# Performance work log

Hardware: AMD Instinct MI355X
Metric: run time of the kernel (lower is better)

The kernel has to match this reference:

```python
import jax, jax.numpy as jnp
import numpy as np

# smoothing constants (from init_kwargs)
KERNEL_SIZE = 20
WINDOW = (-10.0, 10.0)
SIGMA = 4.0
AMPLITUDE = 0.5
N_SMOOTH = 331  # 350 - 20 + 1


def setup_inputs() -> dict:
    key = jax.random.key(0)
    ks = jax.random.split(key, 6)
    W, A, M, D = 4000, 64, 6, 500
    wavelengths = jnp.linspace(0.3, 2.5, W, dtype=jnp.float32)  # um
    grid = jnp.linspace(0.25, 2.6, D, dtype=jnp.float32)        # material wavelength tables
    n_tab = 1.3 + 1.5 * jax.random.uniform(ks[0], (M, D), dtype=jnp.float32)
    k_tab = 0.05 * jax.random.uniform(ks[1], (M, D), dtype=jnp.float32)
    fixed_data = jnp.stack([jnp.broadcast_to(grid, (M, D)), n_tab, k_tab], axis=1)  # [M,3,D]
    refractive_index = 1.5 + 1.5 * jax.random.uniform(ks[2], (350,), dtype=jnp.float32)
    compression_ratio = jnp.ones((1,), jnp.float32)
    thickness_above_unk = 0.05 + 0.2 * jax.random.uniform(ks[3], (10,), dtype=jnp.float32)  # um
    thickness_below_unk = 0.05 + 0.2 * jax.random.uniform(ks[4], (9,), dtype=jnp.float32)   # um
    angle_of_incidences = jnp.linspace(0.0, 60.0, A, dtype=jnp.float32)  # degrees
    # stack order: incoming | 10 above | unknown (index M) | 9 below | outgoing
    md = [0] + [1, 2] * 5 + [M] + [3, 4] * 4 + [3] + [5]
    material_distribution = jnp.array(md, dtype=jnp.int32)  # [22]
    unknown_layer_thickness = jnp.array([500.0], jnp.float32)  # nm
    return dict(refractive_index=refractive_index, compression_ratio=compression_ratio,
                fixed_data=fixed_data, thickness_above_unk=thickness_above_unk,
                thickness_below_unk=thickness_below_unk, wavelengths=wavelengths,
                angle_of_incidences=angle_of_incidences,
                material_distribution=material_distribution, polarization=0,
                unknown_layer_thickness=unknown_layer_thickness)


def reference(refractive_index, compression_ratio, fixed_data, thickness_above_unk,
              thickness_below_unk, wavelengths, angle_of_incidences,
              material_distribution, polarization, unknown_layer_thickness):
    D = fixed_data.shape[2]
    n_repeat = D - N_SMOOTH
    # --- gaussian smoothing of the unknown layer's refractive index (valid conv) ---
    x = jnp.linspace(WINDOW[0], WINDOW[1], KERNEL_SIZE)
    g = AMPLITUDE * jnp.exp(-0.5 * (x / SIGMA) ** 2)
    g = (g / jnp.sum(g)).astype(refractive_index.dtype)
    nk_s = jnp.convolve(refractive_index, g, mode='valid')            # [331]
    nk = jnp.concatenate([nk_s, jnp.full((n_repeat,), nk_s[-1], nk_s.dtype)])  # pad to max_data_dim
    dyn_wl = jnp.linspace(jnp.min(wavelengths), jnp.max(wavelengths), N_SMOOTH)
    dyn_wl = jnp.concatenate([dyn_wl, jnp.full((n_repeat,), dyn_wl[-1], dyn_wl.dtype)])
    # --- interpolate all material n,k tables onto the experimental wavelengths ---
    interp = jax.vmap(lambda xp, fp: jnp.interp(wavelengths, xp, fp))
    n_fixc = interp(fixed_data[:, 0], fixed_data[:, 1]) + 1j * interp(fixed_data[:, 0], fixed_data[:, 2])  # [M,W]
    n_unk = jnp.interp(wavelengths, dyn_wl, nk)[None].astype(n_fixc.dtype)  # unknown layer (k=0)
    n_mat = jnp.concatenate([n_fixc, n_unk], axis=0)                  # [M+1, W]
    n_stack = n_mat[material_distribution]                            # [Lyr, W] complex
    # --- thickness list (unknown in nm -> um, scaled by compression ratio) ---
    d_unk = unknown_layer_thickness / 1000.0 * compression_ratio      # [1]
    d = jnp.concatenate([thickness_above_unk, d_unk, thickness_below_unk])  # [L] = [20]
    # --- coherent TMM, vectorized over (angle, wavelength) ---
    th0 = jnp.deg2rad(angle_of_incidences)                            # [A]
    sin0 = (n_stack[0][None, :] * jnp.sin(th0)[:, None])              # [A,W] (Snell invariant)
    sin_th = sin0[None] / n_stack[:, None, :]                         # [Lyr,A,W]
    cos_th = jnp.sqrt(1.0 - sin_th ** 2)
    kz = 2.0 * jnp.pi * n_stack[:, None, :] * cos_th / wavelengths[None, None, :]
    delta = kz[1:-1] * d[:, None, None].astype(kz.dtype)              # [L,A,W]
    nc = n_stack[:, None, :]
    if polarization == 0:  # s-pol
        f = nc * cos_th                                               # [Lyr,A,W]
        r = (f[:-1] - f[1:]) / (f[:-1] + f[1:])                       # [L+1,A,W]
        t = 2.0 * f[:-1] / (f[:-1] + f[1:])
    else:  # p-pol
        num = nc[1:] * cos_th[:-1]
        den = nc[:-1] * cos_th[1:]
        r = (num - den) / (num + den)
        t = 2.0 * nc[:-1, ] * cos_th[:-1] / (num + den)
    # Mtilde = I_0 * prod_j (P_j @ I_j); 2x2 complex recursion via scan
    m00 = 1.0 / t[0]
    m01 = r[0] / t[0]
    m10 = m01
    m11 = m00

    def step(carry, xs):
        c00, c01, c10, c11 = carry
        dl, rj, tj = xs
        em = jnp.exp(-1j * dl) / tj
        ep = jnp.exp(1j * dl) / tj
        a, b, c, dd = em, rj * em, rj * ep, ep
        return (c00 * a + c01 * c, c00 * b + c01 * dd,
                c10 * a + c11 * c, c10 * b + c11 * dd), None

    (m00, m01, m10, m11), _ = jax.lax.scan(step, (m00, m01, m10, m11), (delta, r[1:], t[1:]))
    rr = m10 / m00
    tt = 1.0 / m00
    R = jnp.abs(rr) ** 2                                              # [A,W]
    if polarization == 0:
        f0 = n_stack[0][None] * cos_th[0]
        ff = n_stack[-1][None] * cos_th[-1]
        T = jnp.abs(tt) ** 2 * jnp.real(ff) / jnp.real(f0)
    else:
        T = (jnp.abs(tt) ** 2 * jnp.real(n_stack[-1][None] * jnp.conj(cos_th[-1]))
             / jnp.real(n_stack[0][None] * jnp.conj(cos_th[0])))
    Aabs = 1.0 - R - T
    return jnp.stack([R, T, Aabs])  # [3, A, W]
```

## Files before the change

kernel.cpp:

```cpp
#include <hip/hip_runtime.h>

#define DEV __device__ __forceinline__
#define RCP(x)  __builtin_amdgcn_rcpf(x)
#define SQRT(x) __builtin_amdgcn_sqrtf(x)

constexpr int W_  = 4000;
constexpr int A_  = 64;
constexpr int D_  = 500;
constexpr int NS_ = 331;
constexpr int KS_ = 20;
constexpr int L_  = 22;
constexpr float PIF = 3.14159265358979323846f;

struct cplx { float re, im; };

DEV cplx cmul(cplx a, cplx b) { return { a.re*b.re - a.im*b.im, a.re*b.im + a.im*b.re }; }
DEV cplx cinv(cplx z) {
  float d = RCP(fmaf(z.re, z.re, z.im * z.im));
  return { z.re * d, -z.im * d };
}
DEV cplx csqrtc(cplx z) {
  float x = z.re, y = z.im;
  float mag = SQRT(fmaf(x, x, y * y));
  float t   = SQRT(0.5f * (mag + fabsf(x)));
  float q   = y * 0.5f * RCP(t);
  bool pos  = (x >= 0.0f);
  float re  = pos ? t : fabsf(q);
  float im  = pos ? q : copysignf(t, y);
  return { re, im };
}

__global__ __launch_bounds__(256) void precompute_kernel(
    const float* __restrict__ ri,
    const float* __restrict__ fixed,
    const float* __restrict__ wl,
    const int*   __restrict__ md,
    float4* __restrict__ nz)
{
  __shared__ float s_grid[D_];
  __shared__ float s_ri[350];
  __shared__ float s_g[KS_];
  __shared__ float s_mn[4], s_mx[4];

  const int tid = threadIdx.x;

  for (int i = tid; i < D_;  i += 256) s_grid[i] = fixed[i];
  for (int i = tid; i < 350; i += 256) s_ri[i]   = ri[i];
  if (tid < KS_) {
    float x  = -10.0f + (float)tid * (20.0f / 19.0f);
    float xs = x * 0.25f;
    s_g[tid] = 0.5f * expf(-0.5f * xs * xs);
  }

  float lmin = 3.4e38f, lmax = -3.4e38f;
  for (int i = tid; i < W_; i += 256) {
    float v = wl[i];
    lmin = fminf(lmin, v); lmax = fmaxf(lmax, v);
  }
  #pragma unroll
  for (int o = 32; o; o >>= 1) {
    lmin = fminf(lmin, __shfl_xor(lmin, o, 64));
    lmax = fmaxf(lmax, __shfl_xor(lmax, o, 64));
  }
  if ((tid & 63) == 0) { s_mn[tid >> 6] = lmin; s_mx[tid >> 6] = lmax; }
  __syncthreads();
  const float wmin = fminf(fminf(s_mn[0], s_mn[1]), fminf(s_mn[2], s_mn[3]));
  const float wmax = fmaxf(fmaxf(s_mx[0], s_mx[1]), fmaxf(s_mx[2], s_mx[3]));

  const int w  = blockIdx.x * 256 + tid;
  const int wc = min(w, W_ - 1);
  const float x = wl[wc];

  cplx nm[7];

  int lo = 0, hi = D_;
  while (lo < hi) { int mid = (lo + hi) >> 1; if (s_grid[mid] <= x) lo = mid + 1; else hi = mid; }
  const int i = min(max(lo, 1), D_ - 1);
  const float gx0 = s_grid[i - 1];
  const float fr  = (x - gx0) * RCP(s_grid[i] - gx0);
  const bool lowc  = (x < s_grid[0]);
  const bool highc = (x > s_grid[D_ - 1]);

  #pragma unroll
  for (int m = 0; m < 6; ++m) {
    const float* nptr = fixed + (m * 3 + 1) * D_;
    const float* kptr = fixed + (m * 3 + 2) * D_;
    float nv = fmaf(fr, nptr[i] - nptr[i - 1], nptr[i - 1]);
    float kv = fmaf(fr, kptr[i] - kptr[i - 1], kptr[i - 1]);
    if (lowc)  { nv = nptr[0];      kv = kptr[0]; }
    if (highc) { nv = nptr[D_ - 1]; kv = kptr[D_ - 1]; }
    nm[m] = { nv, kv };
  }

  {
    float gsum = 0.0f;
    #pragma unroll
    for (int k = 0; k < KS_; ++k) gsum += s_g[k];
    const float ginv  = 1.0f / gsum;
    const float stepd = (wmax - wmin) / (float)(NS_ - 1);
    int j = (int)floorf((x - wmin) * RCP(stepd)) + 1;
    j = min(max(j, 1), NS_ - 1);
    const int j0 = j - 1;
    float a0 = 0.0f, a1 = 0.0f;
    #pragma unroll
    for (int k = 0; k < KS_; ++k) {
      const float gk = s_g[KS_ - 1 - k];
      a0 = fmaf(s_ri[j0 + k], gk, a0);
      a1 = fmaf(s_ri[j0 + 1 + k], gk, a1);
    }
    a0 *= ginv; a1 *= ginv;
    const float d0 = fmaf((float)j0, stepd, wmin);
    const float d1 = fmaf((float)j,  stepd, wmin);
    nm[6] = { fmaf((x - d0) * RCP(d1 - d0), a1 - a0, a0), 0.0f };
  }

  const int m0 = md[0];
  cplx n0 = nm[0];
  #pragma unroll
  for (int m = 1; m < 7; ++m) if (m0 == m) n0 = nm[m];

  if (w < W_) {
    #pragma unroll
    for (int m = 0; m < 7; ++m) {
      const cplx q = cmul(n0, cinv(nm[m]));
      const cplx z = cmul(q, q);
      nz[m * W_ + w] = make_float4(nm[m].re, nm[m].im, z.re, z.im);
    }
  }
}

__global__ __launch_bounds__(256) void tmm_kernel(
    const float4* __restrict__ nz,
    const float*  __restrict__ wl,
    const float*  __restrict__ ang,
    const int*    __restrict__ md,
    const float*  __restrict__ tha,
    const float*  __restrict__ thb,
    const float*  __restrict__ unk,
    const float*  __restrict__ comp,
    float* __restrict__ out)
{
  __shared__ float4 s_f[7 * 256];

  const int tid = threadIdx.x;
  const int w = blockIdx.x * 256 + tid;
  if (w >= W_) return;
  const int a = blockIdx.y;

  const float th0  = ang[a] * (PIF / 180.0f);
  const float s0   = sinf(th0);
  const float s0sq = s0 * s0;
  const float klam = 2.0f * PIF * RCP(wl[w]);

  #pragma unroll
  for (int m = 0; m < 7; ++m) {
    const float4 v = nz[m * W_ + w];
    const cplx st2 = { v.z * s0sq, v.w * s0sq };
    const cplx ct  = csqrtc({ 1.0f - st2.re, -st2.im });
    const cplx f   = cmul({ v.x, v.y }, ct);
    const cplx fi  = cinv(f);
    s_f[m * 256 + tid] = make_float4(f.re, f.im, fi.re, fi.im);
  }

  cplx u   = { 0.0f, 0.0f };
  cplx tac = { 1.0f, 0.0f };
  float4 fdn = s_f[md[L_ - 1] * 256 + tid];
  const float fL_re = fdn.x;

  #pragma unroll
  for (int j = L_ - 2; j >= 1; --j) {
    const float4 fj = s_f[md[j] * 256 + tid];
    const cplx q   = cmul({ fdn.x, fdn.y }, { fj.z, fj.w });
    const cplx iop = cinv({ 1.0f + q.re, q.im });
    const cplx r   = cmul({ 1.0f - q.re, -q.im }, iop);

    const float dthj = (j - 1) < 10 ? tha[j - 1]
                     : ((j - 1) == 10 ? unk[0] / 1000.0f * comp[0]
                                      : thb[j - 12]);
    const float cst = klam * dthj;
    const float dr = fj.x * cst, di = fj.y * cst;
    const float e2 = __expf(-di);
    float sn, cs;
    __sincosf(dr, &sn, &cs);
    const cplx ph   = { e2 * cs, e2 * sn };
    const cplx beta = cmul(ph, ph);

    const cplx ru  = cmul(r, u);
    const cplx idn = cinv({ 1.0f + ru.re, ru.im });
    tac = cmul(tac, cmul(cmul(iop, ph), idn));
    u = cmul(beta, cmul({ r.re + u.re, r.im + u.im }, idn));

    fdn = fj;
  }

  const float4 f0v = s_f[md[0] * 256 + tid];
  const cplx q0   = cmul({ fdn.x, fdn.y }, { f0v.z, f0v.w });
  const cplx iop0 = cinv({ 1.0f + q0.re, q0.im });
  const cplx r0   = cmul({ 1.0f - q0.re, -q0.im }, iop0);
  const cplx ru0  = cmul(r0, u);
  const cplx idn0 = cinv({ 1.0f + ru0.re, ru0.im });
  const cplx rr   = cmul({ r0.re + u.re, r0.im + u.im }, idn0);
  cplx tt = cmul(cmul(iop0, idn0), tac);

  const float SC = 2097152.0f;
  tt.re *= SC; tt.im *= SC;

  const float R = fmaf(rr.re, rr.re, rr.im * rr.im);
  const float T = fmaf(tt.re, tt.re, tt.im * tt.im) * fL_re * RCP(f0v.x);

  const int o = a * W_ + w;
  out[o]               = R;
  out[A_ * W_ + o]     = T;
  out[2 * A_ * W_ + o] = 1.0f - R - T;
}

extern "C" void kernel_launch(void* const* d_in, const int* in_sizes, int n_in,
                              void* d_out, int out_size, void* d_ws, size_t ws_size,
                              hipStream_t stream) {
  const float* ri    = (const float*)d_in[0];
  const float* comp  = (const float*)d_in[1];
  const float* fixed = (const float*)d_in[2];
  const float* tha   = (const float*)d_in[3];
  const float* thb   = (const float*)d_in[4];
  const float* wl    = (const float*)d_in[5];
  const float* ang   = (const float*)d_in[6];
  const int*   md    = (const int*)d_in[7];
  const float* unk   = (const float*)d_in[9];
  float* out = (float*)d_out;

  float4* nz = (float4*)d_ws;

  precompute_kernel<<<16, 256, 0, stream>>>(ri, fixed, wl, md, nz);
  dim3 grid(16, A_);
  tmm_kernel<<<grid, 256, 0, stream>>>(nz, wl, ang, md, tha, thb, unk, comp, out);
}
```

Baseline: 93.04 us.

## Replace per-layer complex division recursion with projective numerator/denominator form

Reformulates the backward reflection recursion so that reflection is carried as a numerator/denominator pair instead of dividing at each layer. This removes one complex inverse per layer. The transmission phase is accumulated as a sum of exponents and applied once at the end, and the interface factors are accumulated in two interleaved products to shorten the dependency chain. The trade is more complex multiplies per layer, plus magnitude scaling tricks that keep the unnormalized numerator and denominator from overflowing, which carries some numerical range risk.

```diff
diff --git a/kernel.cpp b/kernel.cpp
--- a/kernel.cpp
+++ b/kernel.cpp
@@ -15,6 +15,7 @@
 struct cplx { float re, im; };
 
 DEV cplx cmul(cplx a, cplx b) { return { a.re*b.re - a.im*b.im, a.re*b.im + a.im*b.re }; }
+DEV cplx cadd(cplx a, cplx b) { return { a.re + b.re, a.im + b.im }; }
 DEV cplx cinv(cplx z) {
   float d = RCP(fmaf(z.re, z.re, z.im * z.im));
   return { z.re * d, -z.im * d };
@@ -162,8 +163,10 @@
     s_f[m * 256 + tid] = make_float4(f.re, f.im, fi.re, fi.im);
   }
 
-  cplx u   = { 0.0f, 0.0f };
-  cplx tac = { 1.0f, 0.0f };
+  cplx N  = { 0.0f, 0.0f };
+  cplx Dn = { 1.0f, 0.0f };
+  cplx Pa = { 1.0f, 0.0f }, Pb = { 1.0f, 0.0f };
+  float sdr = 0.0f, sabs = 0.0f;
   float4 fdn = s_f[md[L_ - 1] * 256 + tid];
   const float fL_re = fdn.x;
 
@@ -179,16 +182,21 @@
                                       : thb[j - 12]);
     const float cst = klam * dthj;
     const float dr = fj.x * cst, di = fj.y * cst;
-    const float e2 = __expf(-di);
-    float sn, cs;
-    __sincosf(dr, &sn, &cs);
-    const cplx ph   = { e2 * cs, e2 * sn };
-    const cplx beta = cmul(ph, ph);
-
-    const cplx ru  = cmul(r, u);
-    const cplx idn = cinv({ 1.0f + ru.re, ru.im });
-    tac = cmul(tac, cmul(cmul(iop, ph), idn));
-    u = cmul(beta, cmul({ r.re + u.re, r.im + u.im }, idn));
+    sdr += dr; sabs += fabsf(di);
+    const float em = __expf(-2.0f * fabsf(di));
+    const bool dpos = (di >= 0.0f);
+    const float eN = dpos ? em : 1.0f;
+    const float eD = dpos ? 1.0f : em;
+    float sb, cb;
+    __sincosf(2.0f * dr, &sb, &cb);
+    const cplx pN = { eN * cb, eN * sb };
+
+    if (j & 1) Pa = cmul(Pa, iop); else Pb = cmul(Pb, iop);
+
+    const cplx rN = cmul(r, N);
+    const cplx rD = cmul(r, Dn);
+    N  = cmul(pN, cadd(rD, N));
+    Dn = { eD * (Dn.re + rN.re), eD * (Dn.im + rN.im) };
 
     fdn = fj;
   }
@@ -197,13 +205,21 @@
   const cplx q0   = cmul({ fdn.x, fdn.y }, { f0v.z, f0v.w });
   const cplx iop0 = cinv({ 1.0f + q0.re, q0.im });
   const cplx r0   = cmul({ 1.0f - q0.re, -q0.im }, iop0);
-  const cplx ru0  = cmul(r0, u);
-  const cplx idn0 = cinv({ 1.0f + ru0.re, ru0.im });
-  const cplx rr   = cmul({ r0.re + u.re, r0.im + u.im }, idn0);
-  cplx tt = cmul(cmul(iop0, idn0), tac);
-
-  const float SC = 2097152.0f;
-  tt.re *= SC; tt.im *= SC;
+
+  const cplx Nf = cadd(cmul(r0, Dn), N);
+  const cplx Df = cadd(Dn, cmul(r0, N));
+
+  const cplx idf = cinv(Df);
+  const cplx rr  = cmul(Nf, idf);
+
+  const float ei = __expf(-sabs);
+  float ssn, scs;
+  __sincosf(sdr, &ssn, &scs);
+  const cplx phS = { ei * scs, ei * ssn };
+
+  cplx tt = cmul(cmul(iop0, cmul(cmul(Pa, Pb), phS)), idf);
+  const float SCALE = 2097152.0f;
+  tt.re *= SCALE; tt.im *= SCALE;
 
   const float R = fmaf(rr.re, rr.re, rr.im * rr.im);
   const float T = fmaf(tt.re, tt.re, tt.im * tt.im) * fL_re * RCP(f0v.x);
```

New measurement: 91.79 us. About the same (-1.3%).
